# Performance work log

Hardware: AMD Instinct MI355X
Metric: run time of the kernel (lower is better)

## Reference

```python
import jax, jax.numpy as jnp
import numpy as np

B, L = 16, 54            # dialogues, utterances per dialogue
NDIM = 512; H = 512; NS = 2
T = B * L                # 864 utterances
N = 3 * T                # 2592 nodes (l,a,v per utterance)
NE = B * (L + 3)         # 912 hyperedges (3 modality + L utterance per dialogue)
NNZ = 6 * T              # 5184 incidence entries
E = B * 3 * L * (L - 1)  # 137376 directed intra-modality edges
NUM_L = 3; NUM_K = 4
EPS = 1e-8


def _build_indices():
    rng = np.random.default_rng(0)
    spk = rng.integers(0, NS, size=(B, L))
    # qmask [L, B, NS] one-hot of speakers (matches torch argmax path)
    qmask = np.eye(NS, dtype=np.float32)[spk].transpose(1, 0, 2)
    ar = np.arange(L)
    i1, i2, ht = [], [], []
    for d in range(B):
        base = d * 3 * L
        nl = base + ar; na = nl + L; nv = nl + 2 * L
        # 3 modality hyperedges then L per-utterance (l,a,v) hyperedges
        i1 += [nl, na, nv, np.stack([nl, na, nv], 1).reshape(-1)]
        eb = d * (L + 3)
        i2 += [np.repeat(eb + np.arange(3), L), np.repeat(eb + 3 + ar, 3)]
        ht += [np.ones(L, np.int64), np.zeros(3, np.int64)]
    hyperedge_index = np.stack([np.concatenate(i1), np.concatenate(i2)]).astype(np.int64)
    hyperedge_type = np.concatenate(ht)
    # full permutation edges within each modality of each dialogue
    s0 = np.repeat(ar, L); d0 = np.tile(ar, L)
    m = s0 != d0; s0, d0 = s0[m], d0[m]
    src, dst, et = [], [], []
    for d in range(B):
        same = (spk[d][s0] == spk[d][d0]).astype(np.int64)
        for mm in range(3):
            off = d * 3 * L + mm * L
            src.append(s0 + off); dst.append(d0 + off); et.append(same)
    edge_index = np.stack([np.concatenate(src), np.concatenate(dst)]).astype(np.int64)
    edge_type = np.concatenate(et)
    return qmask, hyperedge_index, hyperedge_type, edge_index, edge_type


def setup_inputs() -> dict:
    key = jax.random.key(0)
    ks = jax.random.split(key, 16)
    qmask, hei, het, ei, et = _build_indices()
    n = lambda k, s: jax.random.normal(k, s, dtype=jnp.float32)
    inp = {
        'a': n(ks[0], (T, NDIM)), 'v': n(ks[1], (T, NDIM)), 'l': n(ks[2], (T, NDIM)),
        'qmask': jnp.asarray(qmask),
        'spk_emb': n(ks[3], (NS, NDIM)) * 0.05,
        'fc1_W': n(ks[4], (NDIM, H)) * 0.05, 'fc1_b': jnp.zeros((H,), jnp.float32),
        'he_weight': jnp.ones((NE,), jnp.float32),
        'ew_weight': jnp.ones((NNZ,), jnp.float32),
        'he_attr1': jax.random.uniform(ks[5], (H,), dtype=jnp.float32),
        'he_attr2': jax.random.uniform(ks[6], (H,), dtype=jnp.float32),
        'hc_W': n(ks[7], (NUM_L, H, H)) * 0.05, 'hc_b': jnp.zeros((NUM_L, H), jnp.float32),
        'm3_W0': n(ks[8], (NUM_K, H, H)) * 0.05,
        'm3_W1': n(ks[9], (NUM_K, H, H)) * 0.05,
        'm3_Wself': n(ks[10], (NUM_K, H, H)) * 0.05,
        'm3_b': jnp.zeros((NUM_K, H), jnp.float32),
        'hyperedge_index': jnp.asarray(hei), 'hyperedge_type': jnp.asarray(het),
        'edge_index': jnp.asarray(ei), 'edge_type': jnp.asarray(et),
    }
    return inp


def reference(a, v, l, qmask, spk_emb, fc1_W, fc1_b, he_weight, ew_weight,
              he_attr1, he_attr2, hc_W, hc_b, m3_W0, m3_W1, m3_Wself, m3_b,
              hyperedge_index, hyperedge_type, edge_index, edge_type):
    seg = jax.ops.segment_sum
    # speaker embedding added to text modality (equal dia_len -> simple transpose)
    qm = qmask.transpose(1, 0, 2).reshape(T, NS)
    l = l + spk_emb[jnp.argmax(qm, axis=-1)]
    # per-dialogue node order: [l_d ; a_d ; v_d]
    feats = jnp.concatenate([l.reshape(B, L, NDIM), a.reshape(B, L, NDIM),
                             v.reshape(B, L, NDIM)], axis=1).reshape(N, NDIM)
    x1 = feats @ fc1_W + fc1_b
    node_i, edge_i = hyperedge_index[0], hyperedge_index[1]
    tfl = hyperedge_type.astype(x1.dtype)[:, None]
    edge_attr = he_attr1[None, :] * tfl + he_attr2[None, :] * (1.0 - tfl)  # [NE,H]
    out = x1
    for ll in range(NUM_L):  # hypergraph conv: gather->edge agg->scatter->linear
        de = seg(ew_weight, edge_i, num_segments=NE)
        e = seg(ew_weight[:, None] * out[node_i], edge_i, num_segments=NE)
        e = e / (de + EPS)[:, None] + edge_attr
        c = he_weight[edge_i]
        dn = seg(c, node_i, num_segments=N)
        agg = seg(c[:, None] * e[edge_i], node_i, num_segments=N) / (dn + EPS)[:, None]
        out = jax.nn.relu(agg @ hc_W[ll] + hc_b[ll])
    src, dst = edge_index[0], edge_index[1]
    same_spk = (edge_type == 1)[:, None]
    deg = seg(jnp.ones_like(dst, dtype=x1.dtype), dst, num_segments=N)
    gnn_out = x1
    denoise = jnp.float32(0.0)
    for kk in range(NUM_K):  # 2-relation RGCN-style denoise layer
        h0 = gnn_out @ m3_W0[kk]
        h1 = gnn_out @ m3_W1[kk]
        msg = jnp.where(same_spk, h1[src], h0[src])
        agg = seg(msg, dst, num_segments=N) / (deg + EPS)[:, None]
        f = jax.nn.relu(agg + gnn_out @ m3_Wself[kk] + m3_b[kk])
        denoise = jnp.mean(f * f)
        gnn_out = gnn_out + f
    return out + gnn_out, denoise
```

## Files before the change

kernel.cpp:

```cpp
#include <hip/hip_runtime.h>

typedef unsigned short ushort_t;
typedef __attribute__((ext_vector_type(4))) float f32x4;
typedef __attribute__((ext_vector_type(8))) short s16x8;
typedef __attribute__((ext_vector_type(8))) unsigned short u16x8;

#define NB 16
#define NL 54
#define NT (NB*NL)
#define NNODE (3*NT)
#define NEDGE 912
#define MATSZ (512*512)

__device__ __forceinline__ ushort_t f2b(float f){
  union {unsigned int i; float f;} x; x.f = f;
  unsigned int r = (x.i + 0x7fffu + ((x.i>>16)&1u))>>16;
  return (ushort_t)r;
}

__device__ __forceinline__ void async_copy16(const ushort_t* g, ushort_t* l){
  __builtin_amdgcn_global_load_lds((const __attribute__((address_space(1))) void*)g,
                                   (__attribute__((address_space(3))) void*)l, 16, 0, 0);
}

__global__ __launch_bounds__(256) void transpose_weights(
    const float* __restrict__ fc1, const float* __restrict__ hc,
    const float* __restrict__ m0, const float* __restrict__ m1,
    const float* __restrict__ ms, ushort_t* __restrict__ WT,
    float* __restrict__ acc, unsigned int* __restrict__ counter)
{
  if (blockIdx.x==0 && blockIdx.y==0 && blockIdx.z==0 && threadIdx.x==0){
    *acc = 0.0f; *counter = 0u;
  }
  int w = blockIdx.z;
  const float* src = (w==0) ? fc1
                   : (w<4)  ? hc + (size_t)(w-1)*MATSZ
                   : (w<8)  ? m0 + (size_t)(w-4)*MATSZ
                   : (w<12) ? m1 + (size_t)(w-8)*MATSZ
                            : ms + (size_t)(w-12)*MATSZ;
  ushort_t* dst = WT + (size_t)w*MATSZ;
  __shared__ float tile[64][65];
  int r0 = blockIdx.x*64, c0 = blockIdx.y*64;
  #pragma unroll
  for (int j=0;j<16;j++){
    int idx = j*256 + threadIdx.x;
    int r = idx>>6, c = idx&63;
    tile[r][c] = src[(size_t)(r0+r)*512 + c0 + c];
  }
  __syncthreads();
  #pragma unroll
  for (int j=0;j<16;j++){
    int idx = j*256 + threadIdx.x;
    int r = idx>>6, c = idx&63;
    dst[(size_t)(c0+r)*512 + r0 + c] = f2b(tile[c][r]);
  }
}

template<int AMODE, bool RELU>
__global__ __launch_bounds__(256) void gemm_kernel(
    const float* __restrict__ Afp, const float* __restrict__ Ebuf,
    const float* __restrict__ inA, const float* __restrict__ inV,
    const float* __restrict__ inL, const float* __restrict__ qmask,
    const float* __restrict__ spk_emb, const float* __restrict__ he_w,
    const ushort_t* __restrict__ WT, const float* __restrict__ bias,
    float* __restrict__ C0, float* __restrict__ C1, float* __restrict__ C2,
    int layer)
{
  const int tid = threadIdx.x;
  const int wave = tid>>6, lane = tid&63;
  const int ml = lane&15, quad = lane>>4;
  const int wr = wave>>1, wc = wave&1;
  int row0 = blockIdx.x*64, col0 = blockIdx.y*128;
  int M = NNODE, cst = 512, cbase = 0;
  const ushort_t* Wsel = WT; float* Cout = C0; const float* bsel = bias;
  const float* Asrc = Afp;
  if (AMODE==2){
    int z = blockIdx.z;
    if (z==0){ Wsel = WT + (size_t)(8+layer)*MATSZ; Cout = C0; bsel = nullptr; }
    else if (z==1){ Wsel = WT + (size_t)(12+layer)*MATSZ; Cout = C1; bsel = bias + layer*512; }
    else {
      if (blockIdx.x >= 4) return;
      int colh = blockIdx.x & 1;
      row0 = (blockIdx.x>>1)*64;
      Wsel = WT + (size_t)(4 + colh*4 + layer)*MATSZ;
      Cout = C2; bsel = nullptr; M = 96; cst = 1024; cbase = colh*512;
      Asrc = Ebuf;
    }
  }

  __shared__ __align__(16) ushort_t As[64][80];
  __shared__ __align__(16) ushort_t Bs[128*64];

  const int ar = tid>>3, ac8 = (tid&7)*8;
  const float *sr0=nullptr,*sr1=nullptr,*sp0=nullptr,*sp1=nullptr;
  const float *e10=nullptr,*e20=nullptr,*e11=nullptr,*e21=nullptr;
  float c10=0.f,c20=0.f,c11=0.f,c21=0.f;
  const float *g0=nullptr,*g1=nullptr;
  {
    int n0 = row0+ar;     if (n0 > M-1) n0 = M-1;
    int n1 = row0+ar+32;  if (n1 > M-1) n1 = M-1;
    if (AMODE==0){
      int d=n0/162, rm=n0-d*162, m=rm/54, i=rm-m*54, t=d*54+i;
      sr0 = ((m==0)? inL : (m==1)? inA : inV) + (size_t)t*512;
      if (m==0) sp0 = spk_emb + ((qmask[(i*16+d)*2+1]>qmask[(i*16+d)*2])?512:0);
      d=n1/162; rm=n1-d*162; m=rm/54; i=rm-m*54; t=d*54+i;
      sr1 = ((m==0)? inL : (m==1)? inA : inV) + (size_t)t*512;
      if (m==0) sp1 = spk_emb + ((qmask[(i*16+d)*2+1]>qmask[(i*16+d)*2])?512:0);
    } else if (AMODE==1){
      int d=n0/162, rm=n0-d*162, m=rm/54, i=rm-m*54;
      int em=d*57+m, eu=d*57+3+i;
      float w1=he_w[em], w2=he_w[eu], inv=1.0f/(w1+w2+1e-8f);
      c10=w1*inv; c20=w2*inv; e10=Ebuf+(size_t)em*512; e20=Ebuf+(size_t)eu*512;
      d=n1/162; rm=n1-d*162; m=rm/54; i=rm-m*54;
      em=d*57+m; eu=d*57+3+i;
      w1=he_w[em]; w2=he_w[eu]; inv=1.0f/(w1+w2+1e-8f);
      c11=w1*inv; c21=w2*inv; e11=Ebuf+(size_t)em*512; e21=Ebuf+(size_t)eu*512;
    } else {
      g0 = Asrc + (size_t)n0*512;
      g1 = Asrc + (size_t)n1*512;
    }
  }

  f32x4 acc[2][4];
  #pragma unroll
  for (int mi=0;mi<2;mi++)
    #pragma unroll
    for (int j=0;j<4;j++) acc[mi][j] = (f32x4){0.f,0.f,0.f,0.f};

  const int lr = lane>>3;
  const int lchunk = lane&7;
  const int bswz = (lchunk ^ lr)*8;

  for (int kk=0; kk<512; kk+=64){
    u16x8 av0, av1;
    if (AMODE==0){
      f32x4 xa=*(const f32x4*)(sr0+kk+ac8), xb=*(const f32x4*)(sr0+kk+ac8+4);
      if (sp0){
        f32x4 sa=*(const f32x4*)(sp0+kk+ac8), sb=*(const f32x4*)(sp0+kk+ac8+4);
        #pragma unroll
        for(int j=0;j<4;j++){ xa[j]+=sa[j]; xb[j]+=sb[j]; }
      }
      #pragma unroll
      for(int j=0;j<4;j++){ av0[j]=f2b(xa[j]); av0[4+j]=f2b(xb[j]); }
      xa=*(const f32x4*)(sr1+kk+ac8); xb=*(const f32x4*)(sr1+kk+ac8+4);
      if (sp1){
        f32x4 sa=*(const f32x4*)(sp1+kk+ac8), sb=*(const f32x4*)(sp1+kk+ac8+4);
        #pragma unroll
        for(int j=0;j<4;j++){ xa[j]+=sa[j]; xb[j]+=sb[j]; }
      }
      #pragma unroll
      for(int j=0;j<4;j++){ av1[j]=f2b(xa[j]); av1[4+j]=f2b(xb[j]); }
    } else if (AMODE==1){
      f32x4 xa=*(const f32x4*)(e10+kk+ac8), xb=*(const f32x4*)(e10+kk+ac8+4);
      f32x4 ya=*(const f32x4*)(e20+kk+ac8), yb=*(const f32x4*)(e20+kk+ac8+4);
      #pragma unroll
      for(int j=0;j<4;j++){ av0[j]=f2b(c10*xa[j]+c20*ya[j]); av0[4+j]=f2b(c10*xb[j]+c20*yb[j]); }
      xa=*(const f32x4*)(e11+kk+ac8); xb=*(const f32x4*)(e11+kk+ac8+4);
      ya=*(const f32x4*)(e21+kk+ac8); yb=*(const f32x4*)(e21+kk+ac8+4);
      #pragma unroll
      for(int j=0;j<4;j++){ av1[j]=f2b(c11*xa[j]+c21*ya[j]); av1[4+j]=f2b(c11*xb[j]+c21*yb[j]); }
    } else {
      f32x4 xa=*(const f32x4*)(g0+kk+ac8), xb=*(const f32x4*)(g0+kk+ac8+4);
      #pragma unroll
      for(int j=0;j<4;j++){ av0[j]=f2b(xa[j]); av0[4+j]=f2b(xb[j]); }
      xa=*(const f32x4*)(g1+kk+ac8); xb=*(const f32x4*)(g1+kk+ac8+4);
      #pragma unroll
      for(int j=0;j<4;j++){ av1[j]=f2b(xa[j]); av1[4+j]=f2b(xb[j]); }
    }
    *(u16x8*)&As[ar][ac8]    = av0;
    *(u16x8*)&As[ar+32][ac8] = av1;

    #pragma unroll
    for (int rep=0; rep<4; rep++){
      int bn0 = wave*32 + rep*8;
      const ushort_t* src = Wsel + (size_t)(col0 + bn0 + lr)*512 + kk + bswz;
      async_copy16(src, &Bs[bn0*64]);
    }
    __syncthreads();

    #pragma unroll
    for (int kh=0; kh<2; kh++){
      s16x8 a0 = *(const s16x8*)&As[wr*32 + ml][kh*32 + quad*8];
      s16x8 a1 = *(const s16x8*)&As[wr*32 + 16 + ml][kh*32 + quad*8];
      s16x8 b[4];
      #pragma unroll
      for (int j=0;j<4;j++){
        int bn = wc*64 + j*16 + ml;
        b[j] = *(const s16x8*)&Bs[bn*64 + (((kh*4+quad) ^ (bn&7))<<3)];
      }
      #pragma unroll
      for (int j=0;j<4;j++){
        acc[0][j] = __builtin_amdgcn_mfma_f32_16x16x32_bf16(a0,b[j],acc[0][j],0,0,0);
        acc[1][j] = __builtin_amdgcn_mfma_f32_16x16x32_bf16(a1,b[j],acc[1][j],0,0,0);
      }
    }
    __syncthreads();
  }

  #pragma unroll
  for (int j=0;j<4;j++){
    int wcol = col0 + wc*64 + j*16 + ml;
    float bv = bsel ? bsel[wcol] : 0.f;
    int c = cbase + wcol;
    #pragma unroll
    for (int mi=0;mi<2;mi++){
      int rb = row0 + wr*32 + mi*16 + quad*4;
      f32x4 a = acc[mi][j];
      #pragma unroll
      for (int r=0;r<4;r++){
        int rr = rb + r;
        if (rr < M){
          float v = a[r] + bv;
          if (RELU) v = fmaxf(v, 0.f);
          Cout[(size_t)rr*cst + c] = v;
        }
      }
    }
  }
}

__global__ __launch_bounds__(256) void edge_kernel(const float* __restrict__ X,
    const float* __restrict__ ew, const int* __restrict__ het,
    const float* __restrict__ at1, const float* __restrict__ at2,
    float* __restrict__ E)
{
  int e = blockIdx.x;
  int d = e/57, r = e - d*57;
  int col = threadIdx.x*2;
  float sx=0.f, sy=0.f, de=0.f;
  if (r < 3){
    int nnz0 = d*324 + r*54;
    const float* row = X + ((size_t)(d*162 + r*54))*512 + col;
    for (int i=0;i<54;i++){
      float w = ew[nnz0+i];
      float2 x = *(const float2*)row;
      sx += w*x.x; sy += w*x.y; de += w;
      row += 512;
    }
  } else {
    int i = r-3;
    int nnz0 = d*324 + 162 + i*3;
    #pragma unroll
    for (int m=0;m<3;m++){
      float w = ew[nnz0+m];
      const float* row = X + ((size_t)(d*162 + m*54 + i))*512 + col;
      float2 x = *(const float2*)row;
      sx += w*x.x; sy += w*x.y; de += w;
    }
  }
  float invde = 1.0f/(de + 1e-8f);
  const float* at = het[e] ? at1 : at2;
  float2 o;
  o.x = sx*invde + at[col];
  o.y = sy*invde + at[col+1];
  *(float2*)(E + (size_t)e*512 + col) = o;
}

__global__ __launch_bounds__(256) void gsum_kernel(const float* __restrict__ X,
    const float* __restrict__ qmask, float* __restrict__ Gsum)
{
  int g = blockIdx.x, d = g/3;
  int col = blockIdx.y*256 + threadIdx.x;
  __shared__ unsigned char spks[54];
  if (threadIdx.x < 54){
    int i = threadIdx.x;
    spks[i] = qmask[(i*16+d)*2+1] > qmask[(i*16+d)*2];
  }
  __syncthreads();
  size_t base = (size_t)g*54*512 + col;
  float s0=0.f, s1=0.f;
  for (int i=0;i<54;i++){
    float x = X[base + (size_t)i*512];
    if (spks[i]) s1 += x; else s0 += x;
  }
  Gsum[(size_t)(g*2)*512 + col]   = s0;
  Gsum[(size_t)(g*2+1)*512 + col] = s1;
}

template<bool LAST>
__global__ __launch_bounds__(256) void sf_kernel(
    const float* __restrict__ Gin, const float* __restrict__ H1,
    const float* __restrict__ HS, const float* __restrict__ Sp,
    const float* __restrict__ qmask, float* __restrict__ Gout,
    float* __restrict__ Gsum, const float* __restrict__ OUThg,
    float* __restrict__ dout, float* __restrict__ acc,
    unsigned int* __restrict__ counter)
{
  int g = blockIdx.x, d = g/3;
  int col = blockIdx.y*256 + threadIdx.x;
  __shared__ unsigned char spks[54];
  if (threadIdx.x < 54){
    int i = threadIdx.x;
    spks[i] = qmask[(i*16+d)*2+1] > qmask[(i*16+d)*2];
  }
  __syncthreads();
  const float* r0 = Sp + (size_t)(g*2)*1024;
  const float* r1 = Sp + (size_t)(g*2+1)*1024;
  float S1_0 = r0[512+col];
  float S1_1 = r1[512+col];
  float S0_0 = r1[col];
  float S0_1 = r0[col];
  const float inv = 1.0f/(53.0f + 1e-8f);
  size_t base = (size_t)g*54*512 + col;
  float gs0=0.f, gs1=0.f, sumsq=0.f;
  for (int i=0;i<54;i++){
    size_t off = base + (size_t)i*512;
    int sp = spks[i];
    float S1 = sp ? S1_1 : S1_0;
    float S0 = sp ? S0_1 : S0_0;
    float h1 = H1[off], hs = HS[off], gi = Gin[off];
    float f = fmaxf((S1 - h1 + S0)*inv + hs, 0.f);
    float gn = gi + f;
    Gout[off] = gn;
    if (sp) gs1 += gn; else gs0 += gn;
    if (LAST){
      sumsq += f*f;
      dout[off] = OUThg[off] + gn;
    }
  }
  Gsum[(size_t)(g*2)*512 + col]   = gs0;
  Gsum[(size_t)(g*2+1)*512 + col] = gs1;
  if (LAST){
    __shared__ float red[256];
    red[threadIdx.x] = sumsq;
    __syncthreads();
    #pragma unroll
    for (int s=128; s>0; s>>=1){
      if (threadIdx.x < s) red[threadIdx.x] += red[threadIdx.x+s];
      __syncthreads();
    }
    if (threadIdx.x == 0){
      atomicAdd(acc, red[0]);
      __threadfence();
      unsigned int old = atomicAdd(counter, 1u);
      if (old == 95u){
        float tot = atomicAdd(acc, 0.0f);
        dout[(size_t)NNODE*512] = tot * (1.0f/1327104.0f);
      }
    }
  }
}

extern "C" void kernel_launch(void* const* d_in, const int* in_sizes, int n_in,
                              void* d_out, int out_size, void* d_ws, size_t ws_size,
                              hipStream_t stream)
{
  const float* A_in   = (const float*)d_in[0];
  const float* V_in   = (const float*)d_in[1];
  const float* L_in   = (const float*)d_in[2];
  const float* qmask  = (const float*)d_in[3];
  const float* spk    = (const float*)d_in[4];
  const float* fc1_W  = (const float*)d_in[5];
  const float* fc1_b  = (const float*)d_in[6];
  const float* he_w   = (const float*)d_in[7];
  const float* ew_w   = (const float*)d_in[8];
  const float* attr1  = (const float*)d_in[9];
  const float* attr2  = (const float*)d_in[10];
  const float* hc_W   = (const float*)d_in[11];
  const float* hc_b   = (const float*)d_in[12];
  const float* m3_W0  = (const float*)d_in[13];
  const float* m3_W1  = (const float*)d_in[14];
  const float* m3_Ws  = (const float*)d_in[15];
  const float* m3_b   = (const float*)d_in[16];
  const int*   het    = (const int*)d_in[18];
  float* dout = (float*)d_out;

  char* ws = (char*)d_ws;
  ushort_t* WT = (ushort_t*)ws;
  float* X1   = (float*)(ws + (size_t)16*MATSZ*2);
  float* OUT  = X1  + (size_t)NNODE*512;
  float* H1   = OUT + (size_t)NNODE*512;
  float* HS   = H1  + (size_t)NNODE*512;
  float* G    = HS  + (size_t)NNODE*512;
  float* EB   = G   + (size_t)NNODE*512;
  float* Gsum = EB  + (size_t)NEDGE*512;
  float* Sp   = Gsum + 96*512;
  float* acc  = Sp  + 96*1024;
  unsigned int* counter = (unsigned int*)(acc + 1);

  transpose_weights<<<dim3(8,8,16),256,0,stream>>>(fc1_W, hc_W, m3_W0, m3_W1,
                                                   m3_Ws, WT, acc, counter);

  gemm_kernel<0,false><<<dim3(41,4,1),256,0,stream>>>(
      nullptr, nullptr, A_in, V_in, L_in, qmask, spk, nullptr,
      WT, fc1_b, X1, nullptr, nullptr, 0);

  gsum_kernel<<<dim3(48,2),256,0,stream>>>(X1, qmask, Gsum);

  const float* src = X1;
  for (int ll=0; ll<3; ll++){
    edge_kernel<<<NEDGE,256,0,stream>>>(src, ew_w, het, attr1, attr2, EB);
    gemm_kernel<1,true><<<dim3(41,4,1),256,0,stream>>>(
        nullptr, EB, nullptr, nullptr, nullptr, nullptr, nullptr, he_w,
        WT + (size_t)(1+ll)*MATSZ, hc_b + (size_t)ll*512, OUT, nullptr, nullptr, 0);
    src = OUT;
  }

  for (int kk=0; kk<4; kk++){
    const float* gin = (kk==0) ? X1 : G;
    gemm_kernel<2,false><<<dim3(41,4,3),256,0,stream>>>(
        gin, Gsum, nullptr, nullptr, nullptr, nullptr, nullptr, nullptr,
        WT, m3_b, H1, HS, Sp, kk);
    if (kk<3)
      sf_kernel<false><<<dim3(48,2),256,0,stream>>>(
          gin, H1, HS, Sp, qmask, G, Gsum, nullptr, nullptr, acc, counter);
    else
      sf_kernel<true><<<dim3(48,2),256,0,stream>>>(
          gin, H1, HS, Sp, qmask, G, Gsum, OUT, dout, acc, counter);
  }

  (void)in_sizes; (void)n_in; (void)out_size; (void)ws_size;
}
```

Before: 311.3 us.

## Fold self-edge subtraction into Wself, double-buffer GEMM, fuse gsum into edge kernel

Result: no change. 314.9 us (+1.2%).

```diff
diff --git a/kernel.cpp b/kernel.cpp
--- a/kernel.cpp
+++ b/kernel.cpp
@@ -11,6 +11,7 @@
 #define NNODE (3*NT)
 #define NEDGE 912
 #define MATSZ (512*512)
+#define INV53 (1.0f/(53.0f + 1e-8f))
 
 __device__ __forceinline__ ushort_t f2b(float f){
   union {unsigned int i; float f;} x; x.f = f;
@@ -38,6 +39,7 @@
                    : (w<8)  ? m0 + (size_t)(w-4)*MATSZ
                    : (w<12) ? m1 + (size_t)(w-8)*MATSZ
                             : ms + (size_t)(w-12)*MATSZ;
+  const float* src2 = (w>=12) ? m1 + (size_t)(w-12)*MATSZ : nullptr;
   ushort_t* dst = WT + (size_t)w*MATSZ;
   __shared__ float tile[64][65];
   int r0 = blockIdx.x*64, c0 = blockIdx.y*64;
@@ -45,7 +47,10 @@
   for (int j=0;j<16;j++){
     int idx = j*256 + threadIdx.x;
     int r = idx>>6, c = idx&63;
-    tile[r][c] = src[(size_t)(r0+r)*512 + c0 + c];
+    size_t off = (size_t)(r0+r)*512 + c0 + c;
+    float v = src[off];
+    if (w>=12) v -= INV53 * src2[off];
+    tile[r][c] = v;
   }
   __syncthreads();
   #pragma unroll
@@ -76,8 +81,7 @@
   const float* Asrc = Afp;
   if (AMODE==2){
     int z = blockIdx.z;
-    if (z==0){ Wsel = WT + (size_t)(8+layer)*MATSZ; Cout = C0; bsel = nullptr; }
-    else if (z==1){ Wsel = WT + (size_t)(12+layer)*MATSZ; Cout = C1; bsel = bias + layer*512; }
+    if (z==0){ Wsel = WT + (size_t)(12+layer)*MATSZ; Cout = C0; bsel = bias + layer*512; }
     else {
       if (blockIdx.x >= 4) return;
       int colh = blockIdx.x & 1;
@@ -88,8 +92,8 @@
     }
   }
 
-  __shared__ __align__(16) ushort_t As[64][80];
-  __shared__ __align__(16) ushort_t Bs[128*64];
+  __shared__ __align__(16) ushort_t As[2][64][80];
+  __shared__ __align__(16) ushort_t Bs[2][128*64];
 
   const int ar = tid>>3, ac8 = (tid&7)*8;
   const float *sr0=nullptr,*sr1=nullptr,*sp0=nullptr,*sp1=nullptr;
@@ -131,62 +135,87 @@
   const int lchunk = lane&7;
   const int bswz = (lchunk ^ lr)*8;
 
-  for (int kk=0; kk<512; kk+=64){
+  f32x4 p0a,p0b,p1a,p1b;
+  f32x4 q0a,q0b,q1a,q1b;
+
+  auto loadA = [&](int kk){
+    if (AMODE==0){
+      p0a=*(const f32x4*)(sr0+kk+ac8); p0b=*(const f32x4*)(sr0+kk+ac8+4);
+      if (sp0){ q0a=*(const f32x4*)(sp0+kk+ac8); q0b=*(const f32x4*)(sp0+kk+ac8+4); }
+      p1a=*(const f32x4*)(sr1+kk+ac8); p1b=*(const f32x4*)(sr1+kk+ac8+4);
+      if (sp1){ q1a=*(const f32x4*)(sp1+kk+ac8); q1b=*(const f32x4*)(sp1+kk+ac8+4); }
+    } else if (AMODE==1){
+      p0a=*(const f32x4*)(e10+kk+ac8); p0b=*(const f32x4*)(e10+kk+ac8+4);
+      q0a=*(const f32x4*)(e20+kk+ac8); q0b=*(const f32x4*)(e20+kk+ac8+4);
+      p1a=*(const f32x4*)(e11+kk+ac8); p1b=*(const f32x4*)(e11+kk+ac8+4);
+      q1a=*(const f32x4*)(e21+kk+ac8); q1b=*(const f32x4*)(e21+kk+ac8+4);
+    } else {
+      p0a=*(const f32x4*)(g0+kk+ac8); p0b=*(const f32x4*)(g0+kk+ac8+4);
+      p1a=*(const f32x4*)(g1+kk+ac8); p1b=*(const f32x4*)(g1+kk+ac8+4);
+    }
+  };
+
+  auto cvtWriteA = [&](int buf){
     u16x8 av0, av1;
     if (AMODE==0){
-      f32x4 xa=*(const f32x4*)(sr0+kk+ac8), xb=*(const f32x4*)(sr0+kk+ac8+4);
+      f32x4 xa=p0a, xb=p0b;
       if (sp0){
-        f32x4 sa=*(const f32x4*)(sp0+kk+ac8), sb=*(const f32x4*)(sp0+kk+ac8+4);
         #pragma unroll
-        for(int j=0;j<4;j++){ xa[j]+=sa[j]; xb[j]+=sb[j]; }
+        for(int j=0;j<4;j++){ xa[j]+=q0a[j]; xb[j]+=q0b[j]; }
       }
       #pragma unroll
       for(int j=0;j<4;j++){ av0[j]=f2b(xa[j]); av0[4+j]=f2b(xb[j]); }
-      xa=*(const f32x4*)(sr1+kk+ac8); xb=*(const f32x4*)(sr1+kk+ac8+4);
+      xa=p1a; xb=p1b;
       if (sp1){
-        f32x4 sa=*(const f32x4*)(sp1+kk+ac8), sb=*(const f32x4*)(sp1+kk+ac8+4);
         #pragma unroll
-        for(int j=0;j<4;j++){ xa[j]+=sa[j]; xb[j]+=sb[j]; }
+        for(int j=0;j<4;j++){ xa[j]+=q1a[j]; xb[j]+=q1b[j]; }
       }
       #pragma unroll
       for(int j=0;j<4;j++){ av1[j]=f2b(xa[j]); av1[4+j]=f2b(xb[j]); }
     } else if (AMODE==1){
-      f32x4 xa=*(const f32x4*)(e10+kk+ac8), xb=*(const f32x4*)(e10+kk+ac8+4);
-      f32x4 ya=*(const f32x4*)(e20+kk+ac8), yb=*(const f32x4*)(e20+kk+ac8+4);
-      #pragma unroll
-      for(int j=0;j<4;j++){ av0[j]=f2b(c10*xa[j]+c20*ya[j]); av0[4+j]=f2b(c10*xb[j]+c20*yb[j]); }
-      xa=*(const f32x4*)(e11+kk+ac8); xb=*(const f32x4*)(e11+kk+ac8+4);
-      ya=*(const f32x4*)(e21+kk+ac8); yb=*(const f32x4*)(e21+kk+ac8+4);
-      #pragma unroll
-      for(int j=0;j<4;j++){ av1[j]=f2b(c11*xa[j]+c21*ya[j]); av1[4+j]=f2b(c11*xb[j]+c21*yb[j]); }
+      #pragma unroll
+      for(int j=0;j<4;j++){ av0[j]=f2b(c10*p0a[j]+c20*q0a[j]); av0[4+j]=f2b(c10*p0b[j]+c20*q0b[j]); }
+      #pragma unroll
+      for(int j=0;j<4;j++){ av1[j]=f2b(c11*p1a[j]+c21*q1a[j]); av1[4+j]=f2b(c11*p1b[j]+c21*q1b[j]); }
     } else {
-      f32x4 xa=*(const f32x4*)(g0+kk+ac8), xb=*(const f32x4*)(g0+kk+ac8+4);
-      #pragma unroll
-      for(int j=0;j<4;j++){ av0[j]=f2b(xa[j]); av0[4+j]=f2b(xb[j]); }
-      xa=*(const f32x4*)(g1+kk+ac8); xb=*(const f32x4*)(g1+kk+ac8+4);
-      #pragma unroll
-      for(int j=0;j<4;j++){ av1[j]=f2b(xa[j]); av1[4+j]=f2b(xb[j]); }
-    }
-    *(u16x8*)&As[ar][ac8]    = av0;
-    *(u16x8*)&As[ar+32][ac8] = av1;
-
+      #pragma unroll
+      for(int j=0;j<4;j++){ av0[j]=f2b(p0a[j]); av0[4+j]=f2b(p0b[j]); }
+      #pragma unroll
+      for(int j=0;j<4;j++){ av1[j]=f2b(p1a[j]); av1[4+j]=f2b(p1b[j]); }
+    }
+    *(u16x8*)&As[buf][ar][ac8]    = av0;
+    *(u16x8*)&As[buf][ar+32][ac8] = av1;
+  };
+
+  auto stageB = [&](int buf, int kk){
     #pragma unroll
     for (int rep=0; rep<4; rep++){
       int bn0 = wave*32 + rep*8;
       const ushort_t* src = Wsel + (size_t)(col0 + bn0 + lr)*512 + kk + bswz;
-      async_copy16(src, &Bs[bn0*64]);
-    }
+      async_copy16(src, &Bs[buf][bn0*64]);
+    }
+  };
+
+  loadA(0);
+  stageB(0, 0);
+  cvtWriteA(0);
+
+  int cur = 0;
+  #pragma unroll
+  for (int t=0; t<8; t++){
     __syncthreads();
 
+    if (t<7){ loadA((t+1)*64); stageB(cur^1, (t+1)*64); }
+
     #pragma unroll
     for (int kh=0; kh<2; kh++){
-      s16x8 a0 = *(const s16x8*)&As[wr*32 + ml][kh*32 + quad*8];
-      s16x8 a1 = *(const s16x8*)&As[wr*32 + 16 + ml][kh*32 + quad*8];
+      s16x8 a0 = *(const s16x8*)&As[cur][wr*32 + ml][kh*32 + quad*8];
+      s16x8 a1 = *(const s16x8*)&As[cur][wr*32 + 16 + ml][kh*32 + quad*8];
       s16x8 b[4];
       #pragma unroll
       for (int j=0;j<4;j++){
         int bn = wc*64 + j*16 + ml;
-        b[j] = *(const s16x8*)&Bs[bn*64 + (((kh*4+quad) ^ (bn&7))<<3)];
+        b[j] = *(const s16x8*)&Bs[cur][bn*64 + (((kh*4+quad) ^ (bn&7))<<3)];
       }
       #pragma unroll
       for (int j=0;j<4;j++){
@@ -194,7 +223,9 @@
         acc[1][j] = __builtin_amdgcn_mfma_f32_16x16x32_bf16(a1,b[j],acc[1][j],0,0,0);
       }
     }
-    __syncthreads();
+
+    if (t<7) cvtWriteA(cur^1);
+    cur ^= 1;
   }
 
   #pragma unroll
@@ -219,12 +250,34 @@
   }
 }
 
+template<bool WITHGSUM>
 __global__ __launch_bounds__(256) void edge_kernel(const float* __restrict__ X,
     const float* __restrict__ ew, const int* __restrict__ het,
     const float* __restrict__ at1, const float* __restrict__ at2,
-    float* __restrict__ E)
+    float* __restrict__ E, const float* __restrict__ qmask,
+    float* __restrict__ Gsum)
 {
   int e = blockIdx.x;
+  if (WITHGSUM && e >= NEDGE){
+    int idx = e - NEDGE;
+    int g = idx>>1, d = g/3;
+    int col = (idx&1)*256 + threadIdx.x;
+    __shared__ unsigned char spks[54];
+    if (threadIdx.x < 54){
+      int i = threadIdx.x;
+      spks[i] = qmask[(i*16+d)*2+1] > qmask[(i*16+d)*2];
+    }
+    __syncthreads();
+    size_t base = (size_t)g*54*512 + col;
+    float s0=0.f, s1=0.f;
+    for (int i=0;i<54;i++){
+      float x = X[base + (size_t)i*512];
+      if (spks[i]) s1 += x; else s0 += x;
+    }
+    Gsum[(size_t)(g*2)*512 + col]   = s0;
+    Gsum[(size_t)(g*2+1)*512 + col] = s1;
+    return;
+  }
   int d = e/57, r = e - d*57;
   int col = threadIdx.x*2;
   float sx=0.f, sy=0.f, de=0.f;
@@ -256,8 +309,13 @@
   *(float2*)(E + (size_t)e*512 + col) = o;
 }
 
-__global__ __launch_bounds__(256) void gsum_kernel(const float* __restrict__ X,
-    const float* __restrict__ qmask, float* __restrict__ Gsum)
+template<bool LAST>
+__global__ __launch_bounds__(256) void sf_kernel(
+    const float* __restrict__ Gin, const float* __restrict__ HS,
+    const float* __restrict__ Sp, const float* __restrict__ qmask,
+    float* __restrict__ Gout, float* __restrict__ Gsum,
+    const float* __restrict__ OUThg, float* __restrict__ dout,
+    float* __restrict__ acc, unsigned int* __restrict__ counter)
 {
   int g = blockIdx.x, d = g/3;
   int col = blockIdx.y*256 + threadIdx.x;
@@ -267,40 +325,13 @@
     spks[i] = qmask[(i*16+d)*2+1] > qmask[(i*16+d)*2];
   }
   __syncthreads();
-  size_t base = (size_t)g*54*512 + col;
-  float s0=0.f, s1=0.f;
-  for (int i=0;i<54;i++){
-    float x = X[base + (size_t)i*512];
-    if (spks[i]) s1 += x; else s0 += x;
-  }
-  Gsum[(size_t)(g*2)*512 + col]   = s0;
-  Gsum[(size_t)(g*2+1)*512 + col] = s1;
-}
-
-template<bool LAST>
-__global__ __launch_bounds__(256) void sf_kernel(
-    const float* __restrict__ Gin, const float* __restrict__ H1,
-    const float* __restrict__ HS, const float* __restrict__ Sp,
-    const float* __restrict__ qmask, float* __restrict__ Gout,
-    float* __restrict__ Gsum, const float* __restrict__ OUThg,
-    float* __restrict__ dout, float* __restrict__ acc,
-    unsigned int* __restrict__ counter)
-{
-  int g = blockIdx.x, d = g/3;
-  int col = blockIdx.y*256 + threadIdx.x;
-  __shared__ unsigned char spks[54];
-  if (threadIdx.x < 54){
-    int i = threadIdx.x;
-    spks[i] = qmask[(i*16+d)*2+1] > qmask[(i*16+d)*2];
-  }
-  __syncthreads();
   const float* r0 = Sp + (size_t)(g*2)*1024;
   const float* r1 = Sp + (size_t)(g*2+1)*1024;
   float S1_0 = r0[512+col];
   float S1_1 = r1[512+col];
   float S0_0 = r1[col];
   float S0_1 = r0[col];
-  const float inv = 1.0f/(53.0f + 1e-8f);
+  const float inv = INV53;
   size_t base = (size_t)g*54*512 + col;
   float gs0=0.f, gs1=0.f, sumsq=0.f;
   for (int i=0;i<54;i++){
@@ -308,8 +339,8 @@
     int sp = spks[i];
     float S1 = sp ? S1_1 : S1_0;
     float S0 = sp ? S0_1 : S0_0;
-    float h1 = H1[off], hs = HS[off], gi = Gin[off];
-    float f = fmaxf((S1 - h1 + S0)*inv + hs, 0.f);
+    float hs = HS[off], gi = Gin[off];
+    float f = fmaxf((S1 + S0)*inv + hs, 0.f);
     float gn = gi + f;
     Gout[off] = gn;
     if (sp) gs1 += gn; else gs0 += gn;
@@ -385,11 +416,14 @@
       nullptr, nullptr, A_in, V_in, L_in, qmask, spk, nullptr,
       WT, fc1_b, X1, nullptr, nullptr, 0);
 
-  gsum_kernel<<<dim3(48,2),256,0,stream>>>(X1, qmask, Gsum);
-
   const float* src = X1;
   for (int ll=0; ll<3; ll++){
-    edge_kernel<<<NEDGE,256,0,stream>>>(src, ew_w, het, attr1, attr2, EB);
+    if (ll==0)
+      edge_kernel<true><<<NEDGE+96,256,0,stream>>>(src, ew_w, het, attr1, attr2,
+                                                   EB, qmask, Gsum);
+    else
+      edge_kernel<false><<<NEDGE,256,0,stream>>>(src, ew_w, het, attr1, attr2,
+                                                 EB, nullptr, nullptr);
     gemm_kernel<1,true><<<dim3(41,4,1),256,0,stream>>>(
         nullptr, EB, nullptr, nullptr, nullptr, nullptr, nullptr, he_w,
         WT + (size_t)(1+ll)*MATSZ, hc_b + (size_t)ll*512, OUT, nullptr, nullptr, 0);
@@ -398,15 +432,15 @@
 
   for (int kk=0; kk<4; kk++){
     const float* gin = (kk==0) ? X1 : G;
-    gemm_kernel<2,false><<<dim3(41,4,3),256,0,stream>>>(
+    gemm_kernel<2,false><<<dim3(41,4,2),256,0,stream>>>(
         gin, Gsum, nullptr, nullptr, nullptr, nullptr, nullptr, nullptr,
-        WT, m3_b, H1, HS, Sp, kk);
+        WT, m3_b, HS, nullptr, Sp, kk);
     if (kk<3)
       sf_kernel<false><<<dim3(48,2),256,0,stream>>>(
-          gin, H1, HS, Sp, qmask, G, Gsum, nullptr, nullptr, acc, counter);
+          gin, HS, Sp, qmask, G, Gsum, nullptr, nullptr, acc, counter);
     else
       sf_kernel<true><<<dim3(48,2),256,0,stream>>>(
-          gin, H1, HS, Sp, qmask, G, Gsum, OUT, dout, acc, counter);
+          gin, HS, Sp, qmask, G, Gsum, OUT, dout, acc, counter);
   }
 
   (void)in_sizes; (void)n_in; (void)out_size; (void)ws_size;
```
